# Kernel optimization log

Measured on AMD Instinct MI355X. Metric: run time of the kernel, lower is better.

## Reference

```python
import jax, jax.numpy as jnp
import numpy as np

D_MODEL, D_STATE, D_CONV, EXPAND, HEADDIM = 256, 16, 4, 2, 16
D_INNER = EXPAND * D_MODEL            # 512
NHEADS = D_INNER // HEADDIM           # 32
CONV_DIM = D_INNER + 2 * D_STATE      # 544 (ngroups=1)
D_IN_PROJ = 2 * D_INNER + 2 * D_STATE + NHEADS  # 1088
BATCH, SEQLEN = 8, 4096


def setup_inputs() -> dict:
    key = jax.random.key(0)
    ks = jax.random.split(key, 8)
    u = jax.random.normal(ks[0], (BATCH, SEQLEN, D_MODEL), jnp.float32)
    W_in = jax.random.normal(ks[1], (D_MODEL, D_IN_PROJ), jnp.float32) * 0.02
    conv_w = jax.random.normal(ks[2], (CONV_DIM, 1, D_CONV), jnp.float32) * 0.2
    conv_b = jnp.zeros((CONV_DIM,), jnp.float32)
    # dt_bias init: inverse-softplus of dt ~ Uniform in log-space [dt_min, dt_max]
    dt = jnp.exp(jax.random.uniform(ks[3], (NHEADS,), jnp.float32)
                 * (np.log(0.1) - np.log(0.001)) + np.log(0.001))
    dt = jnp.clip(dt, 1e-4, None)
    dt_bias = dt + jnp.log(-jnp.expm1(-dt))
    A_log = jnp.log(jax.random.uniform(ks[4], (NHEADS,), jnp.float32, 1.0, 16.0))
    D = jnp.ones((NHEADS,), jnp.float32)
    norm_w = jnp.ones((D_INNER,), jnp.float32)
    W_out = jax.random.normal(ks[5], (D_INNER, D_MODEL), jnp.float32) * 0.02
    return dict(u=u, W_in=W_in, conv_w=conv_w, conv_b=conv_b, dt_bias=dt_bias,
                A_log=A_log, D=D, norm_w=norm_w, W_out=W_out)


def _mamba2_forward(u, W_in, conv_w, conv_b, dt_bias, A_log, D, norm_w, W_out):
    batch, seqlen, _ = u.shape
    zxbcdt = u @ W_in                                   # (B, L, 2*d_inner + 2*N + H)
    z = zxbcdt[..., :D_INNER]                           # gate
    xBC = zxbcdt[..., D_INNER:2 * D_INNER + 2 * D_STATE]
    dt = jax.nn.softplus(zxbcdt[..., -NHEADS:] + dt_bias)  # (B, L, H)
    # causal depthwise conv1d over time + SiLU
    xc = jnp.transpose(xBC, (0, 2, 1))                  # (B, C, L)
    xc = jax.lax.conv_general_dilated(
        xc, conv_w, window_strides=(1,), padding=[(D_CONV - 1, 0)],
        feature_group_count=CONV_DIM, dimension_numbers=('NCH', 'OIH', 'NCH'))
    xBC = jax.nn.silu(jnp.transpose(xc, (0, 2, 1)) + conv_b)
    x = xBC[..., :D_INNER].reshape(batch, seqlen, NHEADS, HEADDIM)  # (B,L,H,P)
    Bm = xBC[..., D_INNER:D_INNER + D_STATE]            # (B, L, N), ngroups=1
    Cm = xBC[..., D_INNER + D_STATE:]                   # (B, L, N)
    A = -jnp.exp(A_log)                                 # (H,)
    dA = jnp.exp(dt * A)                                # (B, L, H) decay per step

    # selective scan: h_t = dA_t * h_{t-1} + dt_t * (B_t outer x_t); y_t = C_t . h_t
    def step(h, inp):
        da_t, dt_t, b_t, x_t, c_t = inp
        h = da_t[:, :, None, None] * h + jnp.einsum('bh,bn,bhp->bhpn', dt_t, b_t, x_t)
        y_t = jnp.einsum('bhpn,bn->bhp', h, c_t)
        return h, y_t

    h0 = jnp.zeros((batch, NHEADS, HEADDIM, D_STATE), u.dtype)
    xs = (jnp.moveaxis(dA, 1, 0), jnp.moveaxis(dt, 1, 0),
          jnp.moveaxis(Bm, 1, 0), jnp.moveaxis(x, 1, 0), jnp.moveaxis(Cm, 1, 0))
    _, ys = jax.lax.scan(step, h0, xs)                  # ys: (L, B, H, P)
    y = jnp.moveaxis(ys, 0, 1) + D[None, None, :, None] * x
    y = y.reshape(batch, seqlen, D_INNER)
    # gated RMSNorm (norm_before_gate=False): normalize(y * silu(z)) * weight
    t = y * jax.nn.silu(z)
    t = t * jax.lax.rsqrt(jnp.mean(t * t, axis=-1, keepdims=True) + 1e-5) * norm_w
    return t @ W_out


def reference(u, W_in, conv_w, conv_b, dt_bias, A_log, D, norm_w, W_out):
    return _mamba2_forward(u, W_in, conv_w, conv_b, dt_bias, A_log, D, norm_w, W_out)
```

## Files before the change

### kernel.cpp

```cpp
#include <hip/hip_runtime.h>
#include <hip/hip_bf16.h>
#include <math.h>

#define BATCH   8
#define SEQLEN  4096
#define DMODEL  256
#define DSTATE  16
#define NHEADS  32
#define HEADDIM 16
#define DINNER  512
#define CONVDIM 544
#define DINPROJ 1088
#define NROWS   (BATCH*SEQLEN)
#define CHUNK   64
#define NCH     (SEQLEN/CHUNK)

typedef __attribute__((ext_vector_type(8))) short short8;
typedef __attribute__((ext_vector_type(8))) unsigned short ushort8;
typedef __attribute__((ext_vector_type(4))) float f32x4;

__device__ __forceinline__ float bfu2f(unsigned short u){
  union { float f; unsigned int i; } x; x.i = ((unsigned int)u) << 16; return x.f;
}
__device__ __forceinline__ unsigned short f2bfu(float f){
  union { float f; unsigned int u; } v; v.f = f;
  v.u += 0x7fffu + ((v.u >> 16) & 1u);
  return (unsigned short)(v.u >> 16);
}

__global__ __launch_bounds__(256) void k_cast_u(const float* __restrict__ u, unsigned short* __restrict__ ub){
  int i = blockIdx.x*256 + threadIdx.x;
  float4 v = reinterpret_cast<const float4*>(u)[i];
  ushort4 o; o.x=f2bfu(v.x); o.y=f2bfu(v.y); o.z=f2bfu(v.z); o.w=f2bfu(v.w);
  reinterpret_cast<ushort4*>(ub)[i] = o;
}

__global__ __launch_bounds__(256) void k_transpose_cast(const float* __restrict__ W, unsigned short* __restrict__ WT, int K, int N){
  int idx = blockIdx.x*256 + threadIdx.x;
  if (idx >= N*K) return;
  int n = idx / K, k = idx - n*K;
  WT[idx] = f2bfu(W[(size_t)k*N + n]);
}

template<int EPI, int WC, int K, int NYL2>
__global__ __launch_bounds__(WC*128) void k_gemm(
    const unsigned short* __restrict__ A,
    const unsigned short* __restrict__ BT,
    int nbase,
    unsigned short* __restrict__ oz,
    unsigned short* __restrict__ oxbc,
    float* __restrict__ odtraw,
    float* __restrict__ of32, int Nout)
{
  constexpr int BN      = WC*32;
  constexpr int THREADS = WC*128;
  constexpr int NAI     = 1024/THREADS;
  constexpr int NBI     = (BN*8)/THREADS;
  __shared__ uint4 lds[(128 + BN)*8];
  const int tid = threadIdx.x;
  const int l   = tid & 63;
  const int w   = tid >> 6;
  const int wr  = w & 1, wc = w >> 1;
  int bx, by;
  if (NYL2 == 0){ bx = blockIdx.x; by = 0; }
  else {
    int flat = blockIdx.x;
    int xcd = flat & 7;
    int grp = flat >> 3;
    by = grp & ((1 << NYL2) - 1);
    bx = (grp >> NYL2)*8 + xcd;
  }
  const int bm0 = bx * 128;
  const int bn0 = nbase + by * BN;
  const int fr  = l & 15, kq = l >> 4;
  f32x4 acc[4][2] = {};
  const int nK = K >> 6;
  for (int kt = 0; kt < nK; ++kt){
    const int k0 = kt << 6;
    #pragma unroll
    for (int i = 0; i < NAI; ++i){
      int idx = tid + i*THREADS;
      int row = idx >> 3, slot = idx & 7;
      uint4 v = *reinterpret_cast<const uint4*>(A + (size_t)(bm0+row)*K + k0 + slot*8);
      lds[row*8 + (slot ^ (row & 7))] = v;
    }
    #pragma unroll
    for (int i = 0; i < NBI; ++i){
      int idx = tid + i*THREADS;
      int row = idx >> 3, slot = idx & 7;
      uint4 v = *reinterpret_cast<const uint4*>(BT + (size_t)(bn0+row)*K + k0 + slot*8);
      lds[1024 + row*8 + (slot ^ (row & 7))] = v;
    }
    __syncthreads();
    short8 bf[2][2];
    #pragma unroll
    for (int kk = 0; kk < 2; ++kk){
      #pragma unroll
      for (int nf = 0; nf < 2; ++nf){
        int rb = wc*32 + nf*16 + fr;
        bf[kk][nf] = *reinterpret_cast<const short8*>(&lds[1024 + rb*8 + ((kk*4 + kq) ^ (rb & 7))]);
      }
    }
    #pragma unroll
    for (int mf = 0; mf < 4; ++mf){
      int ra = wr*64 + mf*16 + fr;
      #pragma unroll
      for (int kk = 0; kk < 2; ++kk){
        short8 af = *reinterpret_cast<const short8*>(&lds[ra*8 + ((kk*4 + kq) ^ (ra & 7))]);
        #pragma unroll
        for (int nf = 0; nf < 2; ++nf)
          acc[mf][nf] = __builtin_amdgcn_mfma_f32_16x16x32_bf16(af, bf[kk][nf], acc[mf][nf], 0, 0, 0);
      }
    }
    __syncthreads();
  }
  #pragma unroll
  for (int mf = 0; mf < 4; ++mf){
    #pragma unroll
    for (int nf = 0; nf < 2; ++nf){
      #pragma unroll
      for (int r = 0; r < 4; ++r){
        int m = bm0 + wr*64 + mf*16 + kq*4 + r;
        int n = bn0 + wc*32 + nf*16 + fr;
        float v = acc[mf][nf][r];
        if (EPI == 1){
          if (n < DINNER)                 oz[(size_t)m*DINNER + n] = f2bfu(v);
          else if (n < DINNER + CONVDIM)  oxbc[(size_t)m*CONVDIM + (n - DINNER)] = f2bfu(v);
          else                            odtraw[(size_t)m*NHEADS + (n - DINNER - CONVDIM)] = v;
        } else {
          of32[(size_t)m*Nout + n] = v;
        }
      }
    }
  }
}

__global__ __launch_bounds__(256) void k_convbc(const unsigned short* __restrict__ xbc,
                                                const float* __restrict__ cw,
                                                const float* __restrict__ cb,
                                                float* __restrict__ bco){
  const int tid = threadIdx.x;
  const int j = tid & 31;
  const int rt = tid >> 5;
  const int r0 = blockIdx.x*64 + rt*8;
  const int ch = 512 + j;
  const int tloc = r0 & (SEQLEN-1);
  float wv0 = cw[ch*4+0], wv1 = cw[ch*4+1], wv2 = cw[ch*4+2], wv3 = cw[ch*4+3];
  const float bias = cb[ch];
  float xr[11];
  #pragma unroll
  for (int k = 0; k < 11; ++k){
    int r = r0 - 3 + k;
    xr[k] = (tloc - 3 + k < 0) ? 0.f : bfu2f(xbc[(size_t)r*CONVDIM + ch]);
  }
  #pragma unroll
  for (int i = 0; i < 8; ++i){
    float acc = fmaf(wv0, xr[i], fmaf(wv1, xr[i+1], fmaf(wv2, xr[i+2], fmaf(wv3, xr[i+3], bias))));
    bco[(size_t)(r0+i)*32 + j] = acc / (1.f + __expf(-acc));
  }
}

__global__ __launch_bounds__(256) void k_dtda(const float* __restrict__ dtraw,
                                              const float* __restrict__ dt_bias,
                                              const float* __restrict__ A_log,
                                              float* __restrict__ dt_o,
                                              float* __restrict__ dA_o){
  int i = blockIdx.x*256 + threadIdx.x;
  int h = i & (NHEADS-1);
  float x = dtraw[i] + dt_bias[h];
  float dt = (x > 20.f) ? x : log1pf(expf(x));
  dt_o[i] = dt;
  dA_o[i] = expf(-expf(A_log[h]) * dt);
}

__global__ __launch_bounds__(256,4) void k_scan1(
    const unsigned short* __restrict__ xbc, const float* __restrict__ bc,
    const float* __restrict__ dta, const float* __restrict__ daa,
    const float* __restrict__ cwv, const float* __restrict__ cbv,
    const float* __restrict__ Dv,
    float* __restrict__ yl, float* __restrict__ st, float* __restrict__ Pp)
{
  __shared__ float sBC[65*32];
  __shared__ float sdt[65*16];
  __shared__ float sda[65*16];
  const int tid = threadIdx.x;
  const int bid = blockIdx.x;
  const int qh = bid & 1;
  const int c  = (bid >> 1) & (NCH-1);
  const int b  = bid >> 7;
  const int w  = tid >> 6;
  const int l  = tid & 63;
  const int q  = qh*4 + w;
  const int hh = l >> 4, p = l & 15;
  const int h  = q*4 + hh;
  const size_t row0 = (size_t)b*SEQLEN + (size_t)c*CHUNK;
  const int xoff = q*64 + l;
  {
    const float* src = bc + row0*32;
    #pragma unroll
    for (int i = 0; i < 2; ++i){
      int idx = tid + i*256;
      *reinterpret_cast<float4*>(&sBC[idx*4]) = *reinterpret_cast<const float4*>(src + (size_t)idx*4);
    }
  }
  {
    int t = tid >> 2, g = (tid & 3)*4;
    *reinterpret_cast<float4*>(&sdt[t*16+g]) =
      *reinterpret_cast<const float4*>(dta + (row0+t)*NHEADS + qh*16 + g);
    *reinterpret_cast<float4*>(&sda[t*16+g]) =
      *reinterpret_cast<const float4*>(daa + (row0+t)*NHEADS + qh*16 + g);
  }
  const float cw0 = cwv[xoff*4+0], cw1 = cwv[xoff*4+1], cw2 = cwv[xoff*4+2], cw3 = cwv[xoff*4+3];
  const float cb0 = cbv[xoff];
  const float Dh = Dv[h];
  const int dIdx = w*4 + hh;
  float wA, wB, wC;
  if (c == 0){ wA = wB = wC = 0.f; }
  else {
    wA = bfu2f(xbc[(row0-3)*CONVDIM + xoff]);
    wB = bfu2f(xbc[(row0-2)*CONVDIM + xoff]);
    wC = bfu2f(xbc[(row0-1)*CONVDIM + xoff]);
  }
  float xq0 = bfu2f(xbc[(row0+0)*CONVDIM + xoff]);
  float xq1 = bfu2f(xbc[(row0+1)*CONVDIM + xoff]);
  float xq2 = bfu2f(xbc[(row0+2)*CONVDIM + xoff]);
  float xq3 = bfu2f(xbc[(row0+3)*CONVDIM + xoff]);
  __syncthreads();
  float BA[32], BB[32];
  #pragma unroll
  for (int k = 0; k < 8; ++k)
    *reinterpret_cast<float4*>(&BA[4*k]) = *reinterpret_cast<const float4*>(&sBC[4*k]);
  float dtA = sdt[dIdx], daA = sda[dIdx];
  float dtB, daB;
  float hs[16];
  #pragma unroll
  for (int n = 0; n < 16; ++n) hs[n] = 0.f;
  float cum = 1.f;

#define S1STEP(CUR, NXT, DTC, DAC, DTN, DAN, XQ, T) {                          \
    const int t_ = (T);                                                        \
    _Pragma("unroll")                                                          \
    for (int k = 0; k < 8; ++k)                                                \
      *reinterpret_cast<float4*>(&NXT[4*k]) =                                  \
        *reinterpret_cast<const float4*>(&sBC[(t_+1)*32 + 4*k]);               \
    DTN = sdt[(t_+1)*16 + dIdx]; DAN = sda[(t_+1)*16 + dIdx];                  \
    float xnew = bfu2f(xbc[(row0 + t_ + 4)*CONVDIM + xoff]);                   \
    float xc = fmaf(cw0, wA, fmaf(cw1, wB, fmaf(cw2, wC, fmaf(cw3, XQ, cb0))));\
    wA = wB; wB = wC; wC = XQ; XQ = xnew;                                      \
    float xs = xc / (1.f + __expf(-xc));                                       \
    float dx = DTC * xs;                                                       \
    float y_ = 0.f;                                                            \
    _Pragma("unroll")                                                          \
    for (int n = 0; n < 16; ++n) hs[n] = fmaf(DAC, hs[n], dx*CUR[n]);          \
    _Pragma("unroll")                                                          \
    for (int n = 0; n < 16; ++n) y_ = fmaf(hs[n], CUR[16+n], y_);              \
    cum *= DAC;                                                                \
    yl[(row0 + t_)*DINNER + xoff] = y_ + Dh*xs;                                \
  }

  for (int T = 0; T < CHUNK; T += 4){
    S1STEP(BA, BB, dtA, daA, dtB, daB, xq0, T+0);
    S1STEP(BB, BA, dtB, daB, dtA, daA, xq1, T+1);
    S1STEP(BA, BB, dtA, daA, dtB, daB, xq2, T+2);
    S1STEP(BB, BA, dtB, daB, dtA, daA, xq3, T+3);
  }
#undef S1STEP
  float* sp = st + (((size_t)(b*NHEADS + h)*NCH + c)*16 + p)*16;
  #pragma unroll
  for (int k = 0; k < 4; ++k)
    *reinterpret_cast<float4*>(sp + 4*k) = make_float4(hs[4*k], hs[4*k+1], hs[4*k+2], hs[4*k+3]);
  if (p == 0) Pp[((size_t)b*NHEADS + h)*NCH + c] = cum;
}

__global__ __launch_bounds__(64) void k_scan2(float* __restrict__ st, const float* __restrict__ Pp){
  const int bh = blockIdx.x;
  const int l = threadIdx.x;
  float* sb = st + (size_t)bh*NCH*256 + l*4;
  const float* pb = Pp + (size_t)bh*NCH;
  float4 carry = make_float4(0.f,0.f,0.f,0.f);
  float4 Hb[4]; float Pb[4];
  #pragma unroll
  for (int i = 0; i < 4; ++i){
    Hb[i] = *reinterpret_cast<const float4*>(sb + (size_t)i*256);
    Pb[i] = pb[i];
  }
  for (int c0 = 0; c0 < NCH; c0 += 4){
    #pragma unroll
    for (int i = 0; i < 4; ++i){
      const int cc = c0 + i;
      float4 Hc = Hb[i]; float Pc = Pb[i];
      if (cc + 4 < NCH){
        Hb[i] = *reinterpret_cast<const float4*>(sb + (size_t)(cc+4)*256);
        Pb[i] = pb[cc+4];
      }
      *reinterpret_cast<float4*>(sb + (size_t)cc*256) = carry;
      carry.x = fmaf(Pc, carry.x, Hc.x);
      carry.y = fmaf(Pc, carry.y, Hc.y);
      carry.z = fmaf(Pc, carry.z, Hc.z);
      carry.w = fmaf(Pc, carry.w, Hc.w);
    }
  }
}

__global__ __launch_bounds__(512) void k_scan3g(
    const float* __restrict__ yl, const float* __restrict__ bc,
    const float* __restrict__ daa, const float* __restrict__ st,
    unsigned short* __restrict__ zbf, const float* __restrict__ nw)
{
  __shared__ float sC[65*16];
  __shared__ float sda[65*32];
  __shared__ float sred[2][4][8];
  const int tid = threadIdx.x;
  const int bid = blockIdx.x;
  const int c = bid & (NCH-1);
  const int b = bid >> 6;
  const int w = tid >> 6;
  const int l = tid & 63;
  const int hh = l >> 4, p = l & 15;
  const int h = w*4 + hh;
  const size_t row0 = (size_t)b*SEQLEN + (size_t)c*CHUNK;
  const int xoff = w*64 + l;
  if (tid < 256){
    int t = tid >> 2, g = (tid & 3)*4;
    *reinterpret_cast<float4*>(&sC[t*16+g]) =
      *reinterpret_cast<const float4*>(bc + (row0+t)*32 + 16 + g);
  } else {
    int j = tid - 256;
    #pragma unroll
    for (int kk = 0; kk < 2; ++kk){
      int idx = j*2 + kk;
      int t = idx >> 3, g = (idx & 7)*4;
      *reinterpret_cast<float4*>(&sda[t*32+g]) =
        *reinterpret_cast<const float4*>(daa + (row0+t)*NHEADS + g);
    }
  }
  float hi[16];
  {
    const float* sp = st + (((size_t)(b*NHEADS + h)*NCH + c)*16 + p)*16;
    #pragma unroll
    for (int k = 0; k < 4; ++k){
      float4 v = *reinterpret_cast<const float4*>(sp + 4*k);
      hi[4*k] = v.x; hi[4*k+1] = v.y; hi[4*k+2] = v.z; hi[4*k+3] = v.w;
    }
  }
  const float nwv = nw[xoff];
  float yq0 = yl[(row0+0)*DINNER + xoff];
  float yq1 = yl[(row0+1)*DINNER + xoff];
  float yq2 = yl[(row0+2)*DINNER + xoff];
  float yq3 = yl[(row0+3)*DINNER + xoff];
  float zq0 = bfu2f(zbf[(row0+0)*DINNER + xoff]);
  float zq1 = bfu2f(zbf[(row0+1)*DINNER + xoff]);
  float zq2 = bfu2f(zbf[(row0+2)*DINNER + xoff]);
  float zq3 = bfu2f(zbf[(row0+3)*DINNER + xoff]);
  __syncthreads();
  float CA[16], CB[16];
  #pragma unroll
  for (int k = 0; k < 4; ++k)
    *reinterpret_cast<float4*>(&CA[4*k]) = *reinterpret_cast<const float4*>(&sC[4*k]);
  float daA = sda[h], daB;
  float cum = 1.f;

#define S3STEP(CUR, NXT, DAC, DAN, YQ, ZQ, TV, PS, T) {                        \
    const int t_ = (T);                                                        \
    _Pragma("unroll")                                                          \
    for (int k = 0; k < 4; ++k)                                                \
      *reinterpret_cast<float4*>(&NXT[4*k]) =                                  \
        *reinterpret_cast<const float4*>(&sC[(t_+1)*16 + 4*k]);                \
    DAN = sda[(t_+1)*32 + h];                                                  \
    float ynew = yl[(row0 + t_ + 4)*DINNER + xoff];                            \
    float znew = bfu2f(zbf[(row0 + t_ + 4)*DINNER + xoff]);                    \
    cum *= DAC;                                                                \
    float corr = 0.f;                                                          \
    _Pragma("unroll")                                                          \
    for (int n = 0; n < 16; ++n) corr = fmaf(hi[n], CUR[n], corr);             \
    float yv = YQ + cum*corr;                                                  \
    float sg = ZQ / (1.f + __expf(-ZQ));                                       \
    TV = yv * sg; PS = TV*TV;                                                  \
    YQ = ynew; ZQ = znew;                                                      \
  }

  for (int T = 0; T < CHUNK; T += 4){
    float tv0, tv1, tv2, tv3, ps0, ps1, ps2, ps3;
    S3STEP(CA, CB, daA, daB, yq0, zq0, tv0, ps0, T+0);
    S3STEP(CB, CA, daB, daA, yq1, zq1, tv1, ps1, T+1);
    S3STEP(CA, CB, daA, daB, yq2, zq2, tv2, ps2, T+2);
    S3STEP(CB, CA, daB, daA, yq3, zq3, tv3, ps3, T+3);
    #pragma unroll
    for (int m = 1; m <= 32; m <<= 1){
      ps0 += __shfl_xor(ps0, m, 64);
      ps1 += __shfl_xor(ps1, m, 64);
      ps2 += __shfl_xor(ps2, m, 64);
      ps3 += __shfl_xor(ps3, m, 64);
    }
    const int gb = (T >> 2) & 1;
    if (l == 0){
      sred[gb][0][w] = ps0; sred[gb][1][w] = ps1;
      sred[gb][2][w] = ps2; sred[gb][3][w] = ps3;
    }
    __syncthreads();
    float ss[4];
    #pragma unroll
    for (int i = 0; i < 4; ++i){
      float4 ra = *reinterpret_cast<const float4*>(&sred[gb][i][0]);
      float4 rb = *reinterpret_cast<const float4*>(&sred[gb][i][4]);
      ss[i] = (ra.x+ra.y)+(ra.z+ra.w)+((rb.x+rb.y)+(rb.z+rb.w));
    }
    unsigned short* zp = zbf + (row0 + T)*DINNER + xoff;
    zp[0*DINNER] = f2bfu(tv0 * rsqrtf(ss[0]*(1.f/DINNER) + 1e-5f) * nwv);
    zp[1*DINNER] = f2bfu(tv1 * rsqrtf(ss[1]*(1.f/DINNER) + 1e-5f) * nwv);
    zp[2*DINNER] = f2bfu(tv2 * rsqrtf(ss[2]*(1.f/DINNER) + 1e-5f) * nwv);
    zp[3*DINNER] = f2bfu(tv3 * rsqrtf(ss[3]*(1.f/DINNER) + 1e-5f) * nwv);
  }
#undef S3STEP
}

extern "C" void kernel_launch(void* const* d_in, const int* in_sizes, int n_in,
                              void* d_out, int out_size, void* d_ws, size_t ws_size,
                              hipStream_t stream)
{
  const float* u       = (const float*)d_in[0];
  const float* W_in    = (const float*)d_in[1];
  const float* conv_w  = (const float*)d_in[2];
  const float* conv_b  = (const float*)d_in[3];
  const float* dt_bias = (const float*)d_in[4];
  const float* A_log   = (const float*)d_in[5];
  const float* Dvec    = (const float*)d_in[6];
  const float* norm_w  = (const float*)d_in[7];
  const float* W_out   = (const float*)d_in[8];
  float* out = (float*)d_out;
  char* ws = (char*)d_ws;

  unsigned short* ubf   = (unsigned short*)(ws + 0);
  float* chst           = (float*)(ws + 0);
  unsigned short* wintT = (unsigned short*)(ws + 16777216);
  unsigned short* woutT = (unsigned short*)(ws + 17334272);
  unsigned short* zbf   = (unsigned short*)(ws + 17596416);
  unsigned short* xbcbf = (unsigned short*)(ws + 51150848);
  float* dtraw          = (float*)(ws + 86802432);
  float* Pp             = dtraw;
  float* ylocal         = (float*)(ws + 90996736);
  float* convoBC        = (float*)(ws + 158105600);
  float* dtq            = (float*)(ws + 162299904);
  float* daq            = (float*)(ws + 166494208);

  k_cast_u<<<NROWS*DMODEL/1024, 256, 0, stream>>>(u, ubf);
  k_transpose_cast<<<(DINPROJ*DMODEL+255)/256, 256, 0, stream>>>(W_in, wintT, DMODEL, DINPROJ);
  k_transpose_cast<<<(DINNER*DMODEL+255)/256, 256, 0, stream>>>(W_out, woutT, DINNER, DMODEL);

  k_gemm<1,4,DMODEL,3><<<(NROWS/128)*8, 512, 0, stream>>>(ubf, wintT, 0, zbf, xbcbf, dtraw, nullptr, 0);
  k_gemm<1,2,DMODEL,0><<<NROWS/128, 256, 0, stream>>>(ubf, wintT, 1024, zbf, xbcbf, dtraw, nullptr, 0);

  k_convbc<<<NROWS/64, 256, 0, stream>>>(xbcbf, conv_w, conv_b, convoBC);
  k_dtda<<<NROWS*NHEADS/256, 256, 0, stream>>>(dtraw, dt_bias, A_log, dtq, daq);

  k_scan1<<<BATCH*2*NCH, 256, 0, stream>>>(xbcbf, convoBC, dtq, daq, conv_w, conv_b, Dvec,
                                           ylocal, chst, Pp);
  k_scan2<<<BATCH*NHEADS, 64, 0, stream>>>(chst, Pp);
  k_scan3g<<<BATCH*NCH, 512, 0, stream>>>(ylocal, convoBC, daq, chst, zbf, norm_w);

  k_gemm<2,4,DINNER,1><<<(NROWS/128)*2, 512, 0, stream>>>(zbf, woutT, 0, nullptr, nullptr, nullptr, out, DMODEL);
}
```

Before: 174.7 us.

## Store local scan output in bf16 and split scan3 chunks in half

The intra-chunk scan output y_local is now written as bf16 instead of fp32, halving that intermediate's write and read traffic between scan1 and scan3. scan3 is also split so each block handles half a chunk (32 steps), doubling the grid for more parallelism. The decay prefix is recomputed for the second half with a serial product over the shared da values. bf16 storage of y adds rounding error before the gating and norm.

```diff
diff --git a/kernel.cpp b/kernel.cpp
--- a/kernel.cpp
+++ b/kernel.cpp
@@ -178,7 +178,7 @@
     const float* __restrict__ dta, const float* __restrict__ daa,
     const float* __restrict__ cwv, const float* __restrict__ cbv,
     const float* __restrict__ Dv,
-    float* __restrict__ yl, float* __restrict__ st, float* __restrict__ Pp)
+    unsigned short* __restrict__ ylb, float* __restrict__ st, float* __restrict__ Pp)
 {
   __shared__ float sBC[65*32];
   __shared__ float sdt[65*16];
@@ -255,7 +255,7 @@
     _Pragma("unroll")                                                          \
     for (int n = 0; n < 16; ++n) y_ = fmaf(hs[n], CUR[16+n], y_);              \
     cum *= DAC;                                                                \
-    yl[(row0 + t_)*DINNER + xoff] = y_ + Dh*xs;                                \
+    ylb[(row0 + t_)*DINNER + xoff] = f2bfu(y_ + Dh*xs);                        \
   }
 
   for (int T = 0; T < CHUNK; T += 4){
@@ -303,7 +303,7 @@
 }
 
 __global__ __launch_bounds__(512) void k_scan3g(
-    const float* __restrict__ yl, const float* __restrict__ bc,
+    const unsigned short* __restrict__ ylb, const float* __restrict__ bc,
     const float* __restrict__ daa, const float* __restrict__ st,
     unsigned short* __restrict__ zbf, const float* __restrict__ nw)
 {
@@ -312,8 +312,10 @@
   __shared__ float sred[2][4][8];
   const int tid = threadIdx.x;
   const int bid = blockIdx.x;
-  const int c = bid & (NCH-1);
-  const int b = bid >> 6;
+  const int half = bid & 1;
+  const int c = (bid >> 1) & (NCH-1);
+  const int b = bid >> 7;
+  const int T0 = half*32;
   const int w = tid >> 6;
   const int l = tid & 63;
   const int hh = l >> 4, p = l & 15;
@@ -344,21 +346,22 @@
     }
   }
   const float nwv = nw[xoff];
-  float yq0 = yl[(row0+0)*DINNER + xoff];
-  float yq1 = yl[(row0+1)*DINNER + xoff];
-  float yq2 = yl[(row0+2)*DINNER + xoff];
-  float yq3 = yl[(row0+3)*DINNER + xoff];
-  float zq0 = bfu2f(zbf[(row0+0)*DINNER + xoff]);
-  float zq1 = bfu2f(zbf[(row0+1)*DINNER + xoff]);
-  float zq2 = bfu2f(zbf[(row0+2)*DINNER + xoff]);
-  float zq3 = bfu2f(zbf[(row0+3)*DINNER + xoff]);
+  float yq0 = bfu2f(ylb[(row0+T0+0)*DINNER + xoff]);
+  float yq1 = bfu2f(ylb[(row0+T0+1)*DINNER + xoff]);
+  float yq2 = bfu2f(ylb[(row0+T0+2)*DINNER + xoff]);
+  float yq3 = bfu2f(ylb[(row0+T0+3)*DINNER + xoff]);
+  float zq0 = bfu2f(zbf[(row0+T0+0)*DINNER + xoff]);
+  float zq1 = bfu2f(zbf[(row0+T0+1)*DINNER + xoff]);
+  float zq2 = bfu2f(zbf[(row0+T0+2)*DINNER + xoff]);
+  float zq3 = bfu2f(zbf[(row0+T0+3)*DINNER + xoff]);
   __syncthreads();
+  float cum = 1.f;
+  for (int t = 0; t < T0; ++t) cum *= sda[t*32 + h];
   float CA[16], CB[16];
   #pragma unroll
   for (int k = 0; k < 4; ++k)
-    *reinterpret_cast<float4*>(&CA[4*k]) = *reinterpret_cast<const float4*>(&sC[4*k]);
-  float daA = sda[h], daB;
-  float cum = 1.f;
+    *reinterpret_cast<float4*>(&CA[4*k]) = *reinterpret_cast<const float4*>(&sC[T0*16 + 4*k]);
+  float daA = sda[T0*32 + h], daB;
 
 #define S3STEP(CUR, NXT, DAC, DAN, YQ, ZQ, TV, PS, T) {                        \
     const int t_ = (T);                                                        \
@@ -367,7 +370,7 @@
       *reinterpret_cast<float4*>(&NXT[4*k]) =                                  \
         *reinterpret_cast<const float4*>(&sC[(t_+1)*16 + 4*k]);                \
     DAN = sda[(t_+1)*32 + h];                                                  \
-    float ynew = yl[(row0 + t_ + 4)*DINNER + xoff];                            \
+    float ynew = bfu2f(ylb[(row0 + t_ + 4)*DINNER + xoff]);                    \
     float znew = bfu2f(zbf[(row0 + t_ + 4)*DINNER + xoff]);                    \
     cum *= DAC;                                                                \
     float corr = 0.f;                                                          \
@@ -379,7 +382,7 @@
     YQ = ynew; ZQ = znew;                                                      \
   }
 
-  for (int T = 0; T < CHUNK; T += 4){
+  for (int T = T0; T < T0 + 32; T += 4){
     float tv0, tv1, tv2, tv3, ps0, ps1, ps2, ps3;
     S3STEP(CA, CB, daA, daB, yq0, zq0, tv0, ps0, T+0);
     S3STEP(CB, CA, daB, daA, yq1, zq1, tv1, ps1, T+1);
@@ -438,7 +441,7 @@
   unsigned short* xbcbf = (unsigned short*)(ws + 51150848);
   float* dtraw          = (float*)(ws + 86802432);
   float* Pp             = dtraw;
-  float* ylocal         = (float*)(ws + 90996736);
+  unsigned short* ylb   = (unsigned short*)(ws + 90996736);
   float* convoBC        = (float*)(ws + 158105600);
   float* dtq            = (float*)(ws + 162299904);
   float* daq            = (float*)(ws + 166494208);
@@ -454,9 +457,9 @@
   k_dtda<<<NROWS*NHEADS/256, 256, 0, stream>>>(dtraw, dt_bias, A_log, dtq, daq);
 
   k_scan1<<<BATCH*2*NCH, 256, 0, stream>>>(xbcbf, convoBC, dtq, daq, conv_w, conv_b, Dvec,
-                                           ylocal, chst, Pp);
+                                           ylb, chst, Pp);
   k_scan2<<<BATCH*NHEADS, 64, 0, stream>>>(chst, Pp);
-  k_scan3g<<<BATCH*NCH, 512, 0, stream>>>(ylocal, convoBC, daq, chst, zbf, norm_w);
+  k_scan3g<<<BATCH*NCH*2, 512, 0, stream>>>(ylb, convoBC, daq, chst, zbf, norm_w);
 
   k_gemm<2,4,DINNER,1><<<(NROWS/128)*2, 512, 0, stream>>>(zbf, woutT, 0, nullptr, nullptr, nullptr, out, DMODEL);
 }
```

Result: no change. 174.9 us (+0.1%).
